# Kernel optimization log

Measured on AMD Instinct MI355X. Metric: run time of the kernel, lower is better.

The kernel has to match this reference:

```python
import jax, jax.numpy as jnp
import numpy as np

N = 8388608  # number of histogram bins (2^23)


def setup_inputs() -> dict:
    key = jax.random.key(0)
    # two histograms on the 1D line; emd2 requires equal total mass -> normalize rows
    x = jax.random.uniform(key, (2, N), dtype=jnp.float32)
    x = x / jnp.sum(x, axis=1, keepdims=True)
    return {"x": x}


def reference(x):
    # Exact optimal transport (EMD) between x[0] and x[1] with ground cost
    # M[i,j] = |i - j| (ot.utils.dist on arange(n) with minkowski metric in 1D).
    # For the 1D line metric the exact EMD has the closed form
    #   EMD = sum_i |CDF_a(i) - CDF_b(i)| * (bin spacing = 1)
    # identical to what the network-simplex solver in ot.emd2 returns.
    cdf_diff = jnp.cumsum(x[0] - x[1])  # [n]; last entry ~0 for equal-mass inputs
    return jnp.sum(jnp.abs(cdf_diff))
```

## Files before the change

### kernel.cpp

```cpp
#include <hip/hip_runtime.h>

#define CHUNK 4096
#define BLOCK 256

__device__ __forceinline__ float wave_incl_scan(float v, int lane) {
#pragma unroll
    for (int off = 1; off < 64; off <<= 1) {
        float u = __shfl_up(v, off);
        if (lane >= off) v += u;
    }
    return v;
}

__device__ __forceinline__ float wave_reduce(float v) {
#pragma unroll
    for (int off = 32; off >= 1; off >>= 1) v += __shfl_down(v, off);
    return v;
}

__global__ __launch_bounds__(BLOCK) void k_partial(const float* __restrict__ x0,
                                                   const float* __restrict__ x1,
                                                   float* __restrict__ partials,
                                                   int n) {
    const int t = threadIdx.x;
    const int lane = t & 63;
    const int wave = t >> 6;
    const long base = (long)blockIdx.x * CHUNK;
    float s = 0.f;
#pragma unroll
    for (int k = 0; k < CHUNK / (BLOCK * 4); ++k) {
        long idx = base + (long)(k * BLOCK + t) * 4;
        if (idx + 3 < n) {
            float4 a = *reinterpret_cast<const float4*>(x0 + idx);
            float4 b = *reinterpret_cast<const float4*>(x1 + idx);
            s += (a.x - b.x) + (a.y - b.y) + (a.z - b.z) + (a.w - b.w);
        } else {
#pragma unroll
            for (int j = 0; j < 4; ++j) {
                long i = idx + j;
                if (i < n) s += x0[i] - x1[i];
            }
        }
    }
    s = wave_reduce(s);
    __shared__ float ws[BLOCK / 64];
    if (lane == 0) ws[wave] = s;
    __syncthreads();
    if (t == 0) {
        float tot = 0.f;
#pragma unroll
        for (int w = 0; w < BLOCK / 64; ++w) tot += ws[w];
        partials[blockIdx.x] = tot;
    }
}

__global__ __launch_bounds__(BLOCK) void k_scan(float* __restrict__ partials, int B) {
    const int t = threadIdx.x;
    const int lane = t & 63;
    const int wave = t >> 6;
    const int P = 8;
    float vex[P];
    float run = 0.f;
#pragma unroll
    for (int j = 0; j < P; ++j) {
        int i = t * P + j;
        float x = (i < B) ? partials[i] : 0.f;
        vex[j] = run;
        run += x;
    }
    float tsum = run;
    float inc = wave_incl_scan(tsum, lane);
    __shared__ float wtot[BLOCK / 64];
    if (lane == 63) wtot[wave] = inc;
    __syncthreads();
    float wexcl = 0.f;
    for (int w = 0; w < wave; ++w) wexcl += wtot[w];
    float texcl = wexcl + (inc - tsum);
#pragma unroll
    for (int j = 0; j < P; ++j) {
        int i = t * P + j;
        if (i < B) partials[i] = texcl + vex[j];
    }
}

__global__ __launch_bounds__(BLOCK) void k_emd(const float* __restrict__ x0,
                                               const float* __restrict__ x1,
                                               const float* __restrict__ offsets,
                                               float* __restrict__ out, int n) {
    const int t = threadIdx.x;
    const int lane = t & 63;
    const int wave = t >> 6;
    const long base = (long)blockIdx.x * CHUNK;
    __shared__ float wsum[BLOCK / 64];
    float run = offsets[blockIdx.x];
    float acc = 0.f;
#pragma unroll
    for (int k = 0; k < CHUNK / (BLOCK * 4); ++k) {
        long idx = base + (long)(k * BLOCK + t) * 4;
        float d0 = 0.f, d1 = 0.f, d2 = 0.f, d3 = 0.f;
        int valid = 0;
        if (idx + 3 < n) {
            float4 a = *reinterpret_cast<const float4*>(x0 + idx);
            float4 b = *reinterpret_cast<const float4*>(x1 + idx);
            d0 = a.x - b.x; d1 = a.y - b.y; d2 = a.z - b.z; d3 = a.w - b.w;
            valid = 4;
        } else {
            if (idx + 0 < n) { d0 = x0[idx + 0] - x1[idx + 0]; valid = 1; }
            if (idx + 1 < n) { d1 = x0[idx + 1] - x1[idx + 1]; valid = 2; }
            if (idx + 2 < n) { d2 = x0[idx + 2] - x1[idx + 2]; valid = 3; }
        }
        float p0 = d0, p1 = p0 + d1, p2 = p1 + d2, p3 = p2 + d3;
        float inc = wave_incl_scan(p3, lane);
        if (lane == 63) wsum[wave] = inc;
        __syncthreads();
        float wexcl = 0.f, ctot = 0.f;
#pragma unroll
        for (int w = 0; w < BLOCK / 64; ++w) {
            float x = wsum[w];
            ctot += x;
            if (w < wave) wexcl += x;
        }
        float boff = run + wexcl + (inc - p3);
        if (valid > 0) acc += fabsf(boff + p0);
        if (valid > 1) acc += fabsf(boff + p1);
        if (valid > 2) acc += fabsf(boff + p2);
        if (valid > 3) acc += fabsf(boff + p3);
        run += ctot;
        __syncthreads();
    }
    acc = wave_reduce(acc);
    __shared__ float wacc[BLOCK / 64];
    if (lane == 0) wacc[wave] = acc;
    __syncthreads();
    if (t == 0) {
        float tot = 0.f;
#pragma unroll
        for (int w = 0; w < BLOCK / 64; ++w) tot += wacc[w];
        atomicAdd(out, tot);
    }
}

extern "C" void kernel_launch(void* const* d_in, const int* in_sizes, int n_in,
                              void* d_out, int out_size, void* d_ws, size_t ws_size,
                              hipStream_t stream) {
    const float* x = (const float*)d_in[0];
    const int total = in_sizes[0];
    const int n = total / 2;
    const float* x0 = x;
    const float* x1 = x + n;
    float* out = (float*)d_out;
    float* partials = (float*)d_ws;

    const int B = (n + CHUNK - 1) / CHUNK;

    hipMemsetAsync(out, 0, sizeof(float), stream);
    k_partial<<<B, BLOCK, 0, stream>>>(x0, x1, partials, n);
    k_scan<<<1, BLOCK, 0, stream>>>(partials, B);
    k_emd<<<B, BLOCK, 0, stream>>>(x0, x1, partials, out, n);
}
```

Baseline: 125.8 us.

## Replace three-pass scan with single-pass decoupled look-back scan kernel

Merges the partial-sum, block-scan and EMD kernels into one kernel that uses a dynamic ticket for block ordering and a decoupled look-back over packed flag/value states to get each block's prefix. Each block reads its input from HBM once instead of twice and keeps its chunk in registers, which removes a full second read of both histograms and two kernel launches. In exchange it adds spin-waiting on predecessor blocks, atomics on a state array, an extra memset, and higher register pressure from holding the whole chunk per thread.

```diff
diff --git a/kernel.cpp b/kernel.cpp
--- a/kernel.cpp
+++ b/kernel.cpp
@@ -1,7 +1,10 @@
 #include <hip/hip_runtime.h>
 
+#define BLOCK 256
 #define CHUNK 4096
-#define BLOCK 256
+#define NITER (CHUNK / (BLOCK * 4))
+
+typedef unsigned long long u64;
 
 __device__ __forceinline__ float wave_incl_scan(float v, int lane) {
 #pragma unroll
@@ -18,118 +21,129 @@
     return v;
 }
 
-__global__ __launch_bounds__(BLOCK) void k_partial(const float* __restrict__ x0,
-                                                   const float* __restrict__ x1,
-                                                   float* __restrict__ partials,
-                                                   int n) {
+__device__ __forceinline__ float wave_reduce_bcast(float v) {
+    v = wave_reduce(v);
+    return __shfl(v, 0);
+}
+
+__device__ __forceinline__ u64 pack_state(int flag, float v) {
+    return ((u64)(unsigned)flag << 32) | (u64)__float_as_uint(v);
+}
+
+__global__ __launch_bounds__(BLOCK) void k_emd_onepass(
+    const float* __restrict__ x0, const float* __restrict__ x1,
+    unsigned* __restrict__ ticket, u64* __restrict__ state,
+    float* __restrict__ out, int n) {
     const int t = threadIdx.x;
     const int lane = t & 63;
     const int wave = t >> 6;
-    const long base = (long)blockIdx.x * CHUNK;
-    float s = 0.f;
+
+    __shared__ int s_bid;
+    __shared__ float seg[NITER][BLOCK / 64];
+    __shared__ float s_excl;
+    __shared__ float wacc[BLOCK / 64];
+
+    if (t == 0) s_bid = (int)atomicAdd(ticket, 1u);
+    __syncthreads();
+    const int bid = s_bid;
+    const long base = (long)bid * CHUNK;
+
+    float p[NITER][4];
+    float tincl[NITER];
+
 #pragma unroll
-    for (int k = 0; k < CHUNK / (BLOCK * 4); ++k) {
-        long idx = base + (long)(k * BLOCK + t) * 4;
-        if (idx + 3 < n) {
-            float4 a = *reinterpret_cast<const float4*>(x0 + idx);
-            float4 b = *reinterpret_cast<const float4*>(x1 + idx);
-            s += (a.x - b.x) + (a.y - b.y) + (a.z - b.z) + (a.w - b.w);
-        } else {
-#pragma unroll
-            for (int j = 0; j < 4; ++j) {
-                long i = idx + j;
-                if (i < n) s += x0[i] - x1[i];
-            }
-        }
-    }
-    s = wave_reduce(s);
-    __shared__ float ws[BLOCK / 64];
-    if (lane == 0) ws[wave] = s;
-    __syncthreads();
-    if (t == 0) {
-        float tot = 0.f;
-#pragma unroll
-        for (int w = 0; w < BLOCK / 64; ++w) tot += ws[w];
-        partials[blockIdx.x] = tot;
-    }
-}
-
-__global__ __launch_bounds__(BLOCK) void k_scan(float* __restrict__ partials, int B) {
-    const int t = threadIdx.x;
-    const int lane = t & 63;
-    const int wave = t >> 6;
-    const int P = 8;
-    float vex[P];
-    float run = 0.f;
-#pragma unroll
-    for (int j = 0; j < P; ++j) {
-        int i = t * P + j;
-        float x = (i < B) ? partials[i] : 0.f;
-        vex[j] = run;
-        run += x;
-    }
-    float tsum = run;
-    float inc = wave_incl_scan(tsum, lane);
-    __shared__ float wtot[BLOCK / 64];
-    if (lane == 63) wtot[wave] = inc;
-    __syncthreads();
-    float wexcl = 0.f;
-    for (int w = 0; w < wave; ++w) wexcl += wtot[w];
-    float texcl = wexcl + (inc - tsum);
-#pragma unroll
-    for (int j = 0; j < P; ++j) {
-        int i = t * P + j;
-        if (i < B) partials[i] = texcl + vex[j];
-    }
-}
-
-__global__ __launch_bounds__(BLOCK) void k_emd(const float* __restrict__ x0,
-                                               const float* __restrict__ x1,
-                                               const float* __restrict__ offsets,
-                                               float* __restrict__ out, int n) {
-    const int t = threadIdx.x;
-    const int lane = t & 63;
-    const int wave = t >> 6;
-    const long base = (long)blockIdx.x * CHUNK;
-    __shared__ float wsum[BLOCK / 64];
-    float run = offsets[blockIdx.x];
-    float acc = 0.f;
-#pragma unroll
-    for (int k = 0; k < CHUNK / (BLOCK * 4); ++k) {
+    for (int k = 0; k < NITER; ++k) {
         long idx = base + (long)(k * BLOCK + t) * 4;
         float d0 = 0.f, d1 = 0.f, d2 = 0.f, d3 = 0.f;
-        int valid = 0;
         if (idx + 3 < n) {
             float4 a = *reinterpret_cast<const float4*>(x0 + idx);
             float4 b = *reinterpret_cast<const float4*>(x1 + idx);
             d0 = a.x - b.x; d1 = a.y - b.y; d2 = a.z - b.z; d3 = a.w - b.w;
-            valid = 4;
         } else {
-            if (idx + 0 < n) { d0 = x0[idx + 0] - x1[idx + 0]; valid = 1; }
-            if (idx + 1 < n) { d1 = x0[idx + 1] - x1[idx + 1]; valid = 2; }
-            if (idx + 2 < n) { d2 = x0[idx + 2] - x1[idx + 2]; valid = 3; }
+            if (idx + 0 < n) d0 = x0[idx + 0] - x1[idx + 0];
+            if (idx + 1 < n) d1 = x0[idx + 1] - x1[idx + 1];
+            if (idx + 2 < n) d2 = x0[idx + 2] - x1[idx + 2];
+            if (idx + 3 < n) d3 = x0[idx + 3] - x1[idx + 3];
         }
-        float p0 = d0, p1 = p0 + d1, p2 = p1 + d2, p3 = p2 + d3;
-        float inc = wave_incl_scan(p3, lane);
-        if (lane == 63) wsum[wave] = inc;
-        __syncthreads();
-        float wexcl = 0.f, ctot = 0.f;
+        p[k][0] = d0;
+        p[k][1] = p[k][0] + d1;
+        p[k][2] = p[k][1] + d2;
+        p[k][3] = p[k][2] + d3;
+        float inc = wave_incl_scan(p[k][3], lane);
+        tincl[k] = inc;
+        if (lane == 63) seg[k][wave] = inc;
+    }
+    __syncthreads();
+
+    float offk[NITER];
+    float aggregate = 0.f;
+    {
+        float run = 0.f;
 #pragma unroll
-        for (int w = 0; w < BLOCK / 64; ++w) {
-            float x = wsum[w];
-            ctot += x;
-            if (w < wave) wexcl += x;
+        for (int k = 0; k < NITER; ++k) {
+            float woff = 0.f, ktot = 0.f;
+#pragma unroll
+            for (int w = 0; w < BLOCK / 64; ++w) {
+                float v = seg[k][w];
+                ktot += v;
+                if (w < wave) woff += v;
+            }
+            offk[k] = run + woff;
+            run += ktot;
         }
-        float boff = run + wexcl + (inc - p3);
-        if (valid > 0) acc += fabsf(boff + p0);
-        if (valid > 1) acc += fabsf(boff + p1);
-        if (valid > 2) acc += fabsf(boff + p2);
-        if (valid > 3) acc += fabsf(boff + p3);
-        run += ctot;
-        __syncthreads();
+        aggregate = run;
+    }
+
+    if (t == 0) {
+        __hip_atomic_store(&state[bid], pack_state(1, aggregate),
+                           __ATOMIC_RELEASE, __HIP_MEMORY_SCOPE_AGENT);
+    }
+    if (wave == 0) {
+        float excl = 0.f;
+        int idx = bid - 1;
+        while (idx >= 0) {
+            int look = idx - lane;
+            u64 st = (look >= 0)
+                ? __hip_atomic_load(&state[look], __ATOMIC_ACQUIRE,
+                                    __HIP_MEMORY_SCOPE_AGENT)
+                : pack_state(2, 0.f);
+            int flag = (int)(st >> 32);
+            float val = __uint_as_float((unsigned)st);
+            u64 b2 = __ballot(flag == 2);
+            u64 b0 = __ballot(flag == 0);
+            if (b2) {
+                int pc = __ffsll(b2) - 1;
+                u64 mask = (pc == 0) ? 0ull : ((1ull << pc) - 1ull);
+                if ((b0 & mask) == 0) {
+                    float c = (lane <= pc) ? val : 0.f;
+                    excl += wave_reduce_bcast(c);
+                    break;
+                }
+            } else if (b0 == 0) {
+                excl += wave_reduce_bcast(val);
+                idx -= 64;
+            }
+        }
+        if (lane == 0) {
+            __hip_atomic_store(&state[bid], pack_state(2, excl + aggregate),
+                               __ATOMIC_RELEASE, __HIP_MEMORY_SCOPE_AGENT);
+            s_excl = excl;
+        }
+    }
+    __syncthreads();
+    const float excl = s_excl;
+
+    float acc = 0.f;
+#pragma unroll
+    for (int k = 0; k < NITER; ++k) {
+        long idx = base + (long)(k * BLOCK + t) * 4;
+        float boff = excl + offk[k] + (tincl[k] - p[k][3]);
+        if (idx + 0 < n) acc += fabsf(boff + p[k][0]);
+        if (idx + 1 < n) acc += fabsf(boff + p[k][1]);
+        if (idx + 2 < n) acc += fabsf(boff + p[k][2]);
+        if (idx + 3 < n) acc += fabsf(boff + p[k][3]);
     }
     acc = wave_reduce(acc);
-    __shared__ float wacc[BLOCK / 64];
     if (lane == 0) wacc[wave] = acc;
     __syncthreads();
     if (t == 0) {
@@ -149,12 +163,13 @@
     const float* x0 = x;
     const float* x1 = x + n;
     float* out = (float*)d_out;
-    float* partials = (float*)d_ws;
+
+    unsigned* ticket = (unsigned*)d_ws;
+    u64* state = (u64*)((char*)d_ws + 16);
 
     const int B = (n + CHUNK - 1) / CHUNK;
 
+    hipMemsetAsync(d_ws, 0, 16 + (size_t)B * sizeof(u64), stream);
     hipMemsetAsync(out, 0, sizeof(float), stream);
-    k_partial<<<B, BLOCK, 0, stream>>>(x0, x1, partials, n);
-    k_scan<<<1, BLOCK, 0, stream>>>(partials, B);
-    k_emd<<<B, BLOCK, 0, stream>>>(x0, x1, partials, out, n);
+    k_emd_onepass<<<B, BLOCK, 0, stream>>>(x0, x1, ticket, state, out, n);
 }
```

Measured after the change: 255.7 us. +103.3%, slower.
